# Performance work log

Measured on AMD Instinct MI355X. Metric: run time of the kernel, lower is better.

Reference implementation:

```python
import jax, jax.numpy as jnp
import numpy as np

N = 100000        # nodes
E = 1600000       # edges (avg degree 16)
IN_DIM = 128
OUT_DIM = 128
P_DROP = 0.1


def setup_inputs() -> dict:
    key = jax.random.key(0)
    k1, k2, k3, k4 = jax.random.split(key, 4)
    x = jax.random.normal(k1, (N, IN_DIM), dtype=jnp.float32)
    edge_index = jax.random.randint(k2, (2, E), 0, N, dtype=jnp.int64)
    # glorot-uniform-ish init for the GCNConv linear weight
    limit = float(np.sqrt(6.0 / (IN_DIM + OUT_DIM)))
    W = jax.random.uniform(k3, (IN_DIM, OUT_DIM), dtype=jnp.float32,
                           minval=-limit, maxval=limit)
    b = jnp.zeros((OUT_DIM,), dtype=jnp.float32)
    drop_u = jax.random.uniform(k4, (N, OUT_DIM), dtype=jnp.float32)
    return {"x": x, "edge_index": edge_index, "W": W, "b": b, "drop_u": drop_u}


def reference(x, edge_index, W, b, drop_u):
    n = x.shape[0]
    # linear transform first (PyG GCNConv: lin has no bias)
    h = x @ W  # [N, OUT]
    # add self-loops
    loops = jnp.arange(n, dtype=edge_index.dtype)
    src = jnp.concatenate([edge_index[0], loops])  # [E+N]
    dst = jnp.concatenate([edge_index[1], loops])
    # symmetric normalization: deg computed on destination column
    deg = jax.ops.segment_sum(jnp.ones_like(dst, dtype=h.dtype), dst,
                              num_segments=n)
    dinv = jnp.where(deg > 0, jax.lax.rsqrt(deg), 0.0)
    norm = dinv[src] * dinv[dst]  # [E+N]
    # gather-message-scatter: out[dst] += norm * h[src]
    msgs = h[src] * norm[:, None]                       # [E+N, OUT]
    out = jax.ops.segment_sum(msgs, dst, num_segments=n) + b
    # ReLU + (deterministic-mask) inverted dropout
    out = jax.nn.relu(out)
    keep = 1.0 - P_DROP
    out = jnp.where(drop_u >= P_DROP, out / keep, 0.0)
    return out
```

## Files before the change

### kernel.cpp

```cpp
#include <hip/hip_runtime.h>

#define DIM 128
#define D4 32
#define D2 64
#define EPB1 4096

typedef short short8 __attribute__((ext_vector_type(8)));
typedef float f32x4 __attribute__((ext_vector_type(4)));

__device__ __forceinline__ unsigned pack_bf16(float a, float b) {
    unsigned ua = __float_as_uint(a);
    unsigned ub = __float_as_uint(b);
    ua = (ua + 0x7FFFu + ((ua >> 16) & 1u)) >> 16;
    ub = (ub + 0x7FFFu + ((ub >> 16) & 1u)) & 0xFFFF0000u;
    return ua | ub;
}
__device__ __forceinline__ unsigned short bf16_of(float a) {
    unsigned ua = __float_as_uint(a);
    return (unsigned short)((ua + 0x7FFFu + ((ua >> 16) & 1u)) >> 16);
}
__device__ __forceinline__ float blo(unsigned u) { return __uint_as_float(u << 16); }
__device__ __forceinline__ float bhi(unsigned u) { return __uint_as_float(u & 0xFFFF0000u); }

__device__ __forceinline__ void acc8(const uint4& v,
                                     float& f0, float& f1, float& f2, float& f3,
                                     float& f4, float& f5, float& f6, float& f7) {
    f0 += blo(v.x); f1 += bhi(v.x);
    f2 += blo(v.y); f3 += bhi(v.y);
    f4 += blo(v.z); f5 += bhi(v.z);
    f6 += blo(v.w); f7 += bhi(v.w);
}


__global__ __launch_bounds__(512) void k_hist1(const int* __restrict__ dst, int E,
                                               int* __restrict__ H, int* __restrict__ tot,
                                               int NB1, int NBUCK,
                                               const float* __restrict__ W,
                                               unsigned short* __restrict__ wt) {
    if (blockIdx.x >= (unsigned)NB1) {
        int base = (blockIdx.x - NB1) * 2048 + threadIdx.x * 4;
#pragma unroll
        for (int i = 0; i < 4; ++i) {
            int o = base + i;
            if (o < DIM * DIM) {
                int j = o >> 7, k = o & 127;
                wt[o] = bf16_of(W[k * DIM + j]);
            }
        }
        return;
    }
    __shared__ int h[512];
    const int t = threadIdx.x;
    for (int i = t; i < NBUCK; i += 512) h[i] = 0;
    __syncthreads();
    const int base = blockIdx.x * EPB1;
#pragma unroll
    for (int i = 0; i < EPB1 / 512; ++i) {
        int e = base + i * 512 + t;
        if (e < E) atomicAdd(&h[dst[e] >> 9], 1);
    }
    __syncthreads();
    for (int i = t; i < NBUCK; i += 512) {
        int c = h[i];
        H[i * NB1 + blockIdx.x] = c;
        if (c) atomicAdd(&tot[i], c);
    }
}

__global__ __launch_bounds__(512) void k_scanB(int* __restrict__ H,
                                               const int* __restrict__ tot,
                                               int* __restrict__ binbase,
                                               int NB1, int NBUCK, int E) {
    __shared__ int sh[512];
    const int bin = blockIdx.x;
    const int t = threadIdx.x;

    int tv = (t < NBUCK) ? tot[t] : 0;
    sh[t] = tv;
    __syncthreads();
    for (int o = 1; o < 512; o <<= 1) {
        int x = (t >= o) ? sh[t - o] : 0;
        __syncthreads();
        sh[t] += x;
        __syncthreads();
    }
    const int mybase = sh[bin] - ((bin < NBUCK) ? tot[bin] : 0);
    if (t == bin && t < NBUCK) binbase[t] = mybase;
    if (bin == 0 && t == 0) binbase[NBUCK] = E;
    __syncthreads();

    int v = (t < NB1) ? H[bin * NB1 + t] : 0;
    sh[t] = v;
    __syncthreads();
    for (int o = 1; o < 512; o <<= 1) {
        int x = (t >= o) ? sh[t - o] : 0;
        __syncthreads();
        sh[t] += x;
        __syncthreads();
    }
    if (t < NB1) H[bin * NB1 + t] = mybase + sh[t] - v;
}

__global__ __launch_bounds__(512) void k_scatter1(const int* __restrict__ ei, int E,
                                                  const int* __restrict__ H,
                                                  unsigned* __restrict__ ebuf,
                                                  int NB1, int NBUCK) {
    __shared__ int cnt[512];
    const int t = threadIdx.x;
    const int blk = blockIdx.x;
    for (int i = t; i < NBUCK; i += 512) cnt[i] = 0;
    __syncthreads();
    const int* src = ei;
    const int* dst = ei + E;
    const int base = blk * EPB1;
#pragma unroll
    for (int i = 0; i < EPB1 / 512; ++i) {
        int e = base + i * 512 + t;
        if (e < E) {
            int d = dst[e];
            int s = src[e];
            int b = d >> 9;
            int r = atomicAdd(&cnt[b], 1);
            ebuf[H[b * NB1 + blk] + r] = ((unsigned)s << 9) | (unsigned)(d & 511);
        }
    }
}

__global__ __launch_bounds__(512) void k_bucket2(const unsigned* __restrict__ ebuf,
                                                 const int* __restrict__ binbase,
                                                 int* __restrict__ srclist,
                                                 int* __restrict__ rowstart,
                                                 float* __restrict__ dinv,
                                                 int n, int E) {
    __shared__ int h[512];
    __shared__ int off[512];
    __shared__ int cnt[512];
    const int t = threadIdx.x;
    const int b = blockIdx.x;
    const int beg = binbase[b];
    const int end = binbase[b + 1];
    h[t] = 0; cnt[t] = 0;
    __syncthreads();
    for (int j = beg + t; j < end; j += 512) atomicAdd(&h[ebuf[j] & 511], 1);
    __syncthreads();
    int v = h[t];
    off[t] = v;
    __syncthreads();
    for (int o = 1; o < 512; o <<= 1) {
        int x = (t >= o) ? off[t - o] : 0;
        __syncthreads();
        off[t] += x;
        __syncthreads();
    }
    const int excl = off[t] - v;
    const int node = b * 512 + t;
    if (node < n) {
        rowstart[node] = beg + excl;
        dinv[node] = rsqrtf((float)(v + 1));
    }
    if (b == 0 && t == 0) rowstart[n] = E;
    h[t] = beg + excl;
    __syncthreads();
    for (int j = beg + t; j < end; j += 512) {
        unsigned p = ebuf[j];
        int lo = p & 511;
        int r = atomicAdd(&cnt[lo], 1);
        srclist[h[lo] + r] = (int)(p >> 9);
    }
}


__global__ __launch_bounds__(256) void k_xprep(const float* __restrict__ x,
                                               const float* __restrict__ dinv,
                                               unsigned* __restrict__ xs, int n) {
    long t = (long)blockIdx.x * blockDim.x + threadIdx.x;
    long total = (long)n * D4;
    if (t >= total) return;
    int row = (int)(t >> 5);
    float di = dinv[row];
    float4 v = ((const float4*)x)[t];
    uint2 o;
    o.x = pack_bf16(v.x * di, v.y * di);
    o.y = pack_bf16(v.z * di, v.w * di);
    ((uint2*)xs)[t] = o;
}

__global__ __launch_bounds__(256) void k_wprep(const float* __restrict__ W,
                                               unsigned short* __restrict__ wt) {
    int o = blockIdx.x * blockDim.x + threadIdx.x;
    if (o >= DIM * DIM) return;
    int j = o >> 7, k = o & 127;
    wt[o] = bf16_of(W[k * DIM + j]);
}

__global__ __launch_bounds__(256) void k_gather_bb(const int* __restrict__ rowstart,
                                                   const int* __restrict__ srclist,
                                                   const uint4* __restrict__ xs4,
                                                   const float* __restrict__ dinv,
                                                   uint4* __restrict__ agg4, int n) {
    const int node = blockIdx.x * 4 + (threadIdx.x >> 6);
    const int lane = threadIdx.x & 63;
    if (node >= n) return;
    const int g = lane >> 4;
    const int q = lane & 15;
    const float di = dinv[node];

    float f0 = 0.f, f1 = 0.f, f2 = 0.f, f3 = 0.f,
          f4 = 0.f, f5 = 0.f, f6 = 0.f, f7 = 0.f;
    if (g == 0) {
        uint4 v = xs4[(long)node * 16 + q];
        acc8(v, f0, f1, f2, f3, f4, f5, f6, f7);
    }

    const int beg = rowstart[node];
    const int end = rowstart[node + 1];
    for (int base = beg; base < end; base += 64) {
        const int m = (end - base < 64) ? (end - base) : 64;
        int sidx = (base + lane < end) ? srclist[base + lane] : 0;
        int k = 0;
        for (; k + 8 <= m; k += 8) {
            int sa = __shfl(sidx, k + g);
            int sb = __shfl(sidx, k + 4 + g);
            uint4 va = xs4[(long)sa * 16 + q];
            uint4 vb = xs4[(long)sb * 16 + q];
            acc8(va, f0, f1, f2, f3, f4, f5, f6, f7);
            acc8(vb, f0, f1, f2, f3, f4, f5, f6, f7);
        }
        for (; k + 4 <= m; k += 4) {
            int sa = __shfl(sidx, k + g);
            uint4 va = xs4[(long)sa * 16 + q];
            acc8(va, f0, f1, f2, f3, f4, f5, f6, f7);
        }
        const int rem = m - k;
        if (rem) {
            int sa = __shfl(sidx, k + g);
            if (g < rem) {
                uint4 va = xs4[(long)sa * 16 + q];
                acc8(va, f0, f1, f2, f3, f4, f5, f6, f7);
            }
        }
    }

#pragma unroll
    for (int off = 16; off < 64; off <<= 1) {
        f0 += __shfl_xor(f0, off); f1 += __shfl_xor(f1, off);
        f2 += __shfl_xor(f2, off); f3 += __shfl_xor(f3, off);
        f4 += __shfl_xor(f4, off); f5 += __shfl_xor(f5, off);
        f6 += __shfl_xor(f6, off); f7 += __shfl_xor(f7, off);
    }
    if (g == 0) {
        uint4 o;
        o.x = pack_bf16(f0 * di, f1 * di);
        o.y = pack_bf16(f2 * di, f3 * di);
        o.z = pack_bf16(f4 * di, f5 * di);
        o.w = pack_bf16(f6 * di, f7 * di);
        agg4[(long)node * 16 + q] = o;
    }
}

__global__ __launch_bounds__(256) void k_mfma_transform(
        const unsigned short* __restrict__ A,
        const unsigned short* __restrict__ WT,
        const float* __restrict__ bias,
        const float* __restrict__ du,
        float* __restrict__ out, int n, int ntiles) {
    const int wave  = threadIdx.x >> 6;
    const int lane  = threadIdx.x & 63;
    const int rhalf = wave >> 1;
    const int cg    = wave & 1;
    const int lr    = lane & 15;
    const int g     = lane >> 4;
    const int lk8   = g * 8;

    const int t = blockIdx.x;
    if (t >= ntiles) return;
    const long row0 = (long)t * 32 + rhalf * 16;
    const long grow = row0 + lr;

    long ar = grow; if (ar >= n) ar = n - 1;
    short8 afr[4];
#pragma unroll
    for (int ks = 0; ks < 4; ++ks)
        afr[ks] = *reinterpret_cast<const short8*>(A + ar * DIM + ks * 32 + lk8);

    const float inv_keep = 1.0f / 0.9f;
#pragma unroll
    for (int ct = 0; ct < 4; ++ct) {
        const int colbase = cg * 64 + ct * 16;
        f32x4 acc = {0.f, 0.f, 0.f, 0.f};
#pragma unroll
        for (int ks = 0; ks < 4; ++ks) {
            short8 wfr = *reinterpret_cast<const short8*>(
                WT + (long)(colbase + lr) * DIM + ks * 32 + lk8);
            acc = __builtin_amdgcn_mfma_f32_16x16x32_bf16(wfr, afr[ks], acc, 0, 0, 0);
        }
        if (grow < n) {
            const int gcol = colbase + g * 4;
            float4 bb = *reinterpret_cast<const float4*>(bias + gcol);
            float4 u  = *reinterpret_cast<const float4*>(du + grow * DIM + gcol);
            float4 v;
            v.x = acc[0] + bb.x; v.y = acc[1] + bb.y;
            v.z = acc[2] + bb.z; v.w = acc[3] + bb.w;
            v.x = (u.x >= 0.1f) ? fmaxf(v.x, 0.f) * inv_keep : 0.f;
            v.y = (u.y >= 0.1f) ? fmaxf(v.y, 0.f) * inv_keep : 0.f;
            v.z = (u.z >= 0.1f) ? fmaxf(v.z, 0.f) * inv_keep : 0.f;
            v.w = (u.w >= 0.1f) ? fmaxf(v.w, 0.f) * inv_keep : 0.f;
            *reinterpret_cast<float4*>(out + grow * DIM + gcol) = v;
        }
    }
}


__global__ void k_hist(const int* __restrict__ dst, int E, int* __restrict__ hist) {
    int e = blockIdx.x * blockDim.x + threadIdx.x;
    if (e < E) atomicAdd(&hist[dst[e]], 1);
}
__global__ void k_dinv(const int* __restrict__ hist, float* __restrict__ dinv, int n) {
    int i = blockIdx.x * blockDim.x + threadIdx.x;
    if (i < n) dinv[i] = rsqrtf((float)(hist[i] + 1));
}
__global__ __launch_bounds__(256) void k_scan1(const int* __restrict__ hist,
                                               int* __restrict__ rowstart,
                                               int* __restrict__ bsum, int n) {
    __shared__ int sh[256];
    const int t = threadIdx.x;
    const int base = blockIdx.x * 1024 + t * 4;
    int v0 = (base + 0 < n) ? hist[base + 0] : 0;
    int v1 = (base + 1 < n) ? hist[base + 1] : 0;
    int v2 = (base + 2 < n) ? hist[base + 2] : 0;
    int v3 = (base + 3 < n) ? hist[base + 3] : 0;
    int s = v0 + v1 + v2 + v3;
    sh[t] = s;
    __syncthreads();
    for (int off = 1; off < 256; off <<= 1) {
        int xv = (t >= off) ? sh[t - off] : 0;
        __syncthreads();
        sh[t] += xv;
        __syncthreads();
    }
    if (t == 255) bsum[blockIdx.x] = sh[255];
    int run = sh[t] - s;
    if (base + 0 < n) rowstart[base + 0] = run; run += v0;
    if (base + 1 < n) rowstart[base + 1] = run; run += v1;
    if (base + 2 < n) rowstart[base + 2] = run; run += v2;
    if (base + 3 < n) rowstart[base + 3] = run;
}
__global__ __launch_bounds__(256) void k_scan2(int* __restrict__ bsum, int B) {
    __shared__ int sh[256];
    const int t = threadIdx.x;
    int v = (t < B) ? bsum[t] : 0;
    sh[t] = v;
    __syncthreads();
    for (int off = 1; off < 256; off <<= 1) {
        int xv = (t >= off) ? sh[t - off] : 0;
        __syncthreads();
        sh[t] += xv;
        __syncthreads();
    }
    if (t < B) bsum[t] = sh[t] - v;
}
__global__ void k_scan3(int* __restrict__ rowstart, const int* __restrict__ bsum,
                        int n, int E) {
    int i = blockIdx.x * blockDim.x + threadIdx.x;
    if (i < n) rowstart[i] += bsum[i >> 10];
    else if (i == n) rowstart[n] = E;
}
__global__ void k_fill(const int* __restrict__ ei, int E,
                       const int* __restrict__ rowstart, int* __restrict__ cursor,
                       int* __restrict__ srclist) {
    int e = blockIdx.x * blockDim.x + threadIdx.x;
    if (e >= E) return;
    int d = ei[E + e];
    int pos = atomicAdd(&cursor[d], 1);
    srclist[rowstart[d] + pos] = ei[e];
}
__global__ __launch_bounds__(256) void k_gather_bf(const int* __restrict__ rowstart,
                                                   const int* __restrict__ srclist,
                                                   const unsigned* __restrict__ xs,
                                                   const float* __restrict__ dinv,
                                                   float* __restrict__ out, int n) {
    const int node = blockIdx.x * 4 + (threadIdx.x >> 6);
    const int lane = threadIdx.x & 63;
    if (node >= n) return;
    const float di = dinv[node];
    unsigned sv = xs[(long)node * D2 + lane];
    float2 acc;
    acc.x = __uint_as_float(sv << 16);
    acc.y = __uint_as_float(sv & 0xFFFF0000u);
    const int beg = rowstart[node];
    const int end = rowstart[node + 1];
    int j = beg;
    for (; j + 3 < end; j += 4) {
        int s0 = srclist[j]; int s1 = srclist[j + 1];
        int s2 = srclist[j + 2]; int s3 = srclist[j + 3];
        unsigned v0 = xs[(long)s0 * D2 + lane];
        unsigned v1 = xs[(long)s1 * D2 + lane];
        unsigned v2 = xs[(long)s2 * D2 + lane];
        unsigned v3 = xs[(long)s3 * D2 + lane];
        acc.x += __uint_as_float(v0 << 16) + __uint_as_float(v1 << 16)
               + __uint_as_float(v2 << 16) + __uint_as_float(v3 << 16);
        acc.y += __uint_as_float(v0 & 0xFFFF0000u) + __uint_as_float(v1 & 0xFFFF0000u)
               + __uint_as_float(v2 & 0xFFFF0000u) + __uint_as_float(v3 & 0xFFFF0000u);
    }
    for (; j < end; ++j) {
        unsigned v0 = xs[(long)srclist[j] * D2 + lane];
        acc.x += __uint_as_float(v0 << 16);
        acc.y += __uint_as_float(v0 & 0xFFFF0000u);
    }
    acc.x *= di; acc.y *= di;
    ((float2*)out)[(long)node * D2 + lane] = acc;
}

extern "C" void kernel_launch(void* const* d_in, const int* in_sizes, int n_in,
                              void* d_out, int out_size, void* d_ws, size_t ws_size,
                              hipStream_t stream) {
    const float* x  = (const float*)d_in[0];
    const int*   ei = (const int*)d_in[1];
    const float* W  = (const float*)d_in[2];
    const float* b  = (const float*)d_in[3];
    const float* du = (const float*)d_in[4];
    float* out = (float*)d_out;

    const int n = in_sizes[0] / DIM;
    const int E = in_sizes[1] / 2;

    auto al = [](size_t v) { return (v + 255) & ~(size_t)255; };
    char* ws = (char*)d_ws;

    const int NBUCK = (n + 511) >> 9;
    const int NB1   = (E + EPB1 - 1) / EPB1;

    size_t o_dinv = 0;
    size_t o_rs   = o_dinv + al((size_t)n * 4);
    size_t o_src  = o_rs   + al(((size_t)n + 1) * 4);
    size_t o_xs   = o_src  + al((size_t)E * 4);
    size_t o_agg  = o_xs   + al((size_t)n * DIM * 2);
    size_t o_wt   = o_agg  + al((size_t)n * DIM * 2);
    size_t o_H    = o_wt   + al((size_t)DIM * DIM * 2);
    size_t o_tot  = o_H    + al((size_t)NBUCK * NB1 * 4);
    size_t o_bb   = o_tot  + al((size_t)NBUCK * 4);
    size_t o_ebuf = o_bb   + al(((size_t)NBUCK + 1) * 4);
    size_t need3  = o_ebuf + (size_t)E * 4;

    float* dinv     = (float*)(ws + o_dinv);
    int*   rowstart = (int*)(ws + o_rs);
    int*   srclist  = (int*)(ws + o_src);
    unsigned* xs    = (unsigned*)(ws + o_xs);
    unsigned* agg   = (unsigned*)(ws + o_agg);
    unsigned short* wt = (unsigned short*)(ws + o_wt);
    int*   H        = (int*)(ws + o_H);
    int*   tot      = (int*)(ws + o_tot);
    int*   binbase  = (int*)(ws + o_bb);
    unsigned* ebuf  = (unsigned*)(ws + o_ebuf);

    const int bs = 256;

    if (ws_size >= need3 && NBUCK <= 512 && NB1 <= 512) {
        (void)hipMemsetAsync(tot, 0, (size_t)NBUCK * 4, stream);
        k_hist1<<<NB1 + 8, 512, 0, stream>>>(ei + E, E, H, tot, NB1, NBUCK, W, wt);
        k_scanB<<<NBUCK, 512, 0, stream>>>(H, tot, binbase, NB1, NBUCK, E);
        k_scatter1<<<NB1, 512, 0, stream>>>(ei, E, H, ebuf, NB1, NBUCK);
        k_bucket2<<<NBUCK, 512, 0, stream>>>(ebuf, binbase, srclist, rowstart, dinv, n, E);

        long t_x = (long)n * D4;
        k_xprep<<<(int)((t_x + bs - 1) / bs), bs, 0, stream>>>(x, dinv, xs, n);
        k_gather_bb<<<(n + 3) / 4, 256, 0, stream>>>(rowstart, srclist,
                                                     (const uint4*)xs, dinv,
                                                     (uint4*)agg, n);
        int ntiles = (n + 31) / 32;
        k_mfma_transform<<<ntiles, 256, 0, stream>>>((const unsigned short*)agg, wt,
                                                     b, du, out, n, ntiles);
        return;
    }

    size_t f_dinv = 0;
    size_t f_hist = f_dinv + al((size_t)n * 4);
    size_t f_rs   = f_hist + al((size_t)n * 4);
    size_t f_bsum = f_rs   + al(((size_t)n + 1) * 4);
    size_t f_src  = f_bsum + 1024;
    size_t f_xs   = f_src  + al((size_t)E * 4);
    size_t f_agg  = f_xs   + al((size_t)n * DIM * 2);
    size_t f_wt   = f_agg  + al((size_t)n * DIM * 2);
    size_t need1  = f_agg;
    size_t need2  = f_wt + (size_t)DIM * DIM * 2;

    float* fdinv     = (float*)(ws + f_dinv);
    int*   fhist     = (int*)(ws + f_hist);
    int*   frowstart = (int*)(ws + f_rs);
    int*   fbsum     = (int*)(ws + f_bsum);
    int*   fsrclist  = (int*)(ws + f_src);
    unsigned* fxs    = (unsigned*)(ws + f_xs);
    unsigned* fagg   = (unsigned*)(ws + f_agg);
    unsigned short* fwt = (unsigned short*)(ws + f_wt);

    const int B = (n + 1023) / 1024;
    (void)hipMemsetAsync(fhist, 0, (size_t)n * 4, stream);
    k_hist<<<(E + bs - 1) / bs, bs, 0, stream>>>(ei + E, E, fhist);
    k_dinv<<<(n + bs - 1) / bs, bs, 0, stream>>>(fhist, fdinv, n);
    k_scan1<<<B, 256, 0, stream>>>(fhist, frowstart, fbsum, n);
    k_scan2<<<1, 256, 0, stream>>>(fbsum, B);
    k_scan3<<<(n + 1 + bs - 1) / bs, bs, 0, stream>>>(frowstart, fbsum, n, E);
    (void)hipMemsetAsync(fhist, 0, (size_t)n * 4, stream);
    k_fill<<<(E + bs - 1) / bs, bs, 0, stream>>>(ei, E, frowstart, fhist, fsrclist);

    if (ws_size >= need2) {
        long t_x = (long)n * D4;
        k_xprep<<<(int)((t_x + bs - 1) / bs), bs, 0, stream>>>(x, fdinv, fxs, n);
        k_wprep<<<(DIM * DIM + bs - 1) / bs, bs, 0, stream>>>(W, fwt);
        k_gather_bb<<<(n + 3) / 4, 256, 0, stream>>>(frowstart, fsrclist,
                                                     (const uint4*)fxs, fdinv,
                                                     (uint4*)fagg, n);
        int ntiles = (n + 31) / 32;
        k_mfma_transform<<<ntiles, 256, 0, stream>>>((const unsigned short*)fagg, fwt,
                                                     b, du, out, n, ntiles);
    } else if (ws_size >= need1) {
        long t_x = (long)n * D4;
        k_xprep<<<(int)((t_x + bs - 1) / bs), bs, 0, stream>>>(x, fdinv, fxs, n);
        k_gather_bf<<<(n + 3) / 4, 256, 0, stream>>>(frowstart, fsrclist, fxs, fdinv, out, n);
    }
}
```

Measured before the change: 169.1 us.

## Fuse neighbor gather and MFMA transform into one kernel via LDS tile

```diff
diff --git a/kernel.cpp b/kernel.cpp
--- a/kernel.cpp
+++ b/kernel.cpp
@@ -193,95 +193,94 @@
     wt[o] = bf16_of(W[k * DIM + j]);
 }
 
-__global__ __launch_bounds__(256) void k_gather_bb(const int* __restrict__ rowstart,
-                                                   const int* __restrict__ srclist,
-                                                   const uint4* __restrict__ xs4,
-                                                   const float* __restrict__ dinv,
-                                                   uint4* __restrict__ agg4, int n) {
-    const int node = blockIdx.x * 4 + (threadIdx.x >> 6);
+__global__ __launch_bounds__(256) void k_gather_mfma(
+        const int* __restrict__ rowstart, const int* __restrict__ srclist,
+        const uint4* __restrict__ xs4, const float* __restrict__ dinv,
+        const unsigned short* __restrict__ WT, const float* __restrict__ bias,
+        const float* __restrict__ du, float* __restrict__ out,
+        int n, int ntiles) {
+    __shared__ unsigned char Atile[32 * 256];
+
+    const int wv   = threadIdx.x >> 6;
     const int lane = threadIdx.x & 63;
-    if (node >= n) return;
     const int g = lane >> 4;
     const int q = lane & 15;
-    const float di = dinv[node];
-
-    float f0 = 0.f, f1 = 0.f, f2 = 0.f, f3 = 0.f,
-          f4 = 0.f, f5 = 0.f, f6 = 0.f, f7 = 0.f;
-    if (g == 0) {
-        uint4 v = xs4[(long)node * 16 + q];
-        acc8(v, f0, f1, f2, f3, f4, f5, f6, f7);
-    }
-
-    const int beg = rowstart[node];
-    const int end = rowstart[node + 1];
-    for (int base = beg; base < end; base += 64) {
-        const int m = (end - base < 64) ? (end - base) : 64;
-        int sidx = (base + lane < end) ? srclist[base + lane] : 0;
-        int k = 0;
-        for (; k + 8 <= m; k += 8) {
-            int sa = __shfl(sidx, k + g);
-            int sb = __shfl(sidx, k + 4 + g);
-            uint4 va = xs4[(long)sa * 16 + q];
-            uint4 vb = xs4[(long)sb * 16 + q];
-            acc8(va, f0, f1, f2, f3, f4, f5, f6, f7);
-            acc8(vb, f0, f1, f2, f3, f4, f5, f6, f7);
-        }
-        for (; k + 4 <= m; k += 4) {
-            int sa = __shfl(sidx, k + g);
-            uint4 va = xs4[(long)sa * 16 + q];
-            acc8(va, f0, f1, f2, f3, f4, f5, f6, f7);
-        }
-        const int rem = m - k;
-        if (rem) {
-            int sa = __shfl(sidx, k + g);
-            if (g < rem) {
-                uint4 va = xs4[(long)sa * 16 + q];
-                acc8(va, f0, f1, f2, f3, f4, f5, f6, f7);
+    const long row0 = (long)blockIdx.x * 32;
+
+    for (int nd = 0; nd < 8; ++nd) {
+        const int lrow = wv * 8 + nd;
+        const long node = row0 + lrow;
+        unsigned char* dstb = Atile + lrow * 256 + ((q * 16) ^ ((lrow & 7) << 4));
+        if (node < n) {
+            const float di = dinv[node];
+            float f0 = 0.f, f1 = 0.f, f2 = 0.f, f3 = 0.f,
+                  f4 = 0.f, f5 = 0.f, f6 = 0.f, f7 = 0.f;
+            if (g == 0) {
+                uint4 v = xs4[node * 16 + q];
+                acc8(v, f0, f1, f2, f3, f4, f5, f6, f7);
             }
-        }
-    }
-
-#pragma unroll
-    for (int off = 16; off < 64; off <<= 1) {
-        f0 += __shfl_xor(f0, off); f1 += __shfl_xor(f1, off);
-        f2 += __shfl_xor(f2, off); f3 += __shfl_xor(f3, off);
-        f4 += __shfl_xor(f4, off); f5 += __shfl_xor(f5, off);
-        f6 += __shfl_xor(f6, off); f7 += __shfl_xor(f7, off);
-    }
-    if (g == 0) {
-        uint4 o;
-        o.x = pack_bf16(f0 * di, f1 * di);
-        o.y = pack_bf16(f2 * di, f3 * di);
-        o.z = pack_bf16(f4 * di, f5 * di);
-        o.w = pack_bf16(f6 * di, f7 * di);
-        agg4[(long)node * 16 + q] = o;
-    }
-}
-
-__global__ __launch_bounds__(256) void k_mfma_transform(
-        const unsigned short* __restrict__ A,
-        const unsigned short* __restrict__ WT,
-        const float* __restrict__ bias,
-        const float* __restrict__ du,
-        float* __restrict__ out, int n, int ntiles) {
-    const int wave  = threadIdx.x >> 6;
-    const int lane  = threadIdx.x & 63;
-    const int rhalf = wave >> 1;
-    const int cg    = wave & 1;
+            const int beg = rowstart[node];
+            const int end = rowstart[node + 1];
+            for (int base = beg; base < end; base += 64) {
+                const int m = (end - base < 64) ? (end - base) : 64;
+                int sidx = (base + lane < end) ? srclist[base + lane] : 0;
+                int k = 0;
+                for (; k + 8 <= m; k += 8) {
+                    int sa = __shfl(sidx, k + g);
+                    int sb = __shfl(sidx, k + 4 + g);
+                    uint4 va = xs4[(long)sa * 16 + q];
+                    uint4 vb = xs4[(long)sb * 16 + q];
+                    acc8(va, f0, f1, f2, f3, f4, f5, f6, f7);
+                    acc8(vb, f0, f1, f2, f3, f4, f5, f6, f7);
+                }
+                for (; k + 4 <= m; k += 4) {
+                    int sa = __shfl(sidx, k + g);
+                    uint4 va = xs4[(long)sa * 16 + q];
+                    acc8(va, f0, f1, f2, f3, f4, f5, f6, f7);
+                }
+                const int rem = m - k;
+                if (rem) {
+                    int sa = __shfl(sidx, k + g);
+                    if (g < rem) {
+                        uint4 va = xs4[(long)sa * 16 + q];
+                        acc8(va, f0, f1, f2, f3, f4, f5, f6, f7);
+                    }
+                }
+            }
+#pragma unroll
+            for (int off = 16; off < 64; off <<= 1) {
+                f0 += __shfl_xor(f0, off); f1 += __shfl_xor(f1, off);
+                f2 += __shfl_xor(f2, off); f3 += __shfl_xor(f3, off);
+                f4 += __shfl_xor(f4, off); f5 += __shfl_xor(f5, off);
+                f6 += __shfl_xor(f6, off); f7 += __shfl_xor(f7, off);
+            }
+            if (g == 0) {
+                uint4 o;
+                o.x = pack_bf16(f0 * di, f1 * di);
+                o.y = pack_bf16(f2 * di, f3 * di);
+                o.z = pack_bf16(f4 * di, f5 * di);
+                o.w = pack_bf16(f6 * di, f7 * di);
+                *(uint4*)dstb = o;
+            }
+        } else if (g == 0) {
+            uint4 z; z.x = z.y = z.z = z.w = 0u;
+            *(uint4*)dstb = z;
+        }
+    }
+    __syncthreads();
+
+    const int rhalf = wv >> 1;
+    const int cg    = wv & 1;
     const int lr    = lane & 15;
-    const int g     = lane >> 4;
     const int lk8   = g * 8;
-
-    const int t = blockIdx.x;
-    if (t >= ntiles) return;
-    const long row0 = (long)t * 32 + rhalf * 16;
-    const long grow = row0 + lr;
-
-    long ar = grow; if (ar >= n) ar = n - 1;
+    const int lrowA = rhalf * 16 + lr;
+    const long grow = row0 + lrowA;
+
     short8 afr[4];
 #pragma unroll
     for (int ks = 0; ks < 4; ++ks)
-        afr[ks] = *reinterpret_cast<const short8*>(A + ar * DIM + ks * 32 + lk8);
+        afr[ks] = *(const short8*)(Atile + lrowA * 256 +
+                                   (((ks * 64) + g * 16) ^ ((lrowA & 7) << 4)));
 
     const float inv_keep = 1.0f / 0.9f;
 #pragma unroll
@@ -411,6 +410,119 @@
     ((float2*)out)[(long)node * D2 + lane] = acc;
 }
 
+__global__ __launch_bounds__(256) void k_gather_bb(const int* __restrict__ rowstart,
+                                                   const int* __restrict__ srclist,
+                                                   const uint4* __restrict__ xs4,
+                                                   const float* __restrict__ dinv,
+                                                   uint4* __restrict__ agg4, int n) {
+    const int node = blockIdx.x * 4 + (threadIdx.x >> 6);
+    const int lane = threadIdx.x & 63;
+    if (node >= n) return;
+    const int g = lane >> 4;
+    const int q = lane & 15;
+    const float di = dinv[node];
+
+    float f0 = 0.f, f1 = 0.f, f2 = 0.f, f3 = 0.f,
+          f4 = 0.f, f5 = 0.f, f6 = 0.f, f7 = 0.f;
+    if (g == 0) {
+        uint4 v = xs4[(long)node * 16 + q];
+        acc8(v, f0, f1, f2, f3, f4, f5, f6, f7);
+    }
+    const int beg = rowstart[node];
+    const int end = rowstart[node + 1];
+    for (int base = beg; base < end; base += 64) {
+        const int m = (end - base < 64) ? (end - base) : 64;
+        int sidx = (base + lane < end) ? srclist[base + lane] : 0;
+        int k = 0;
+        for (; k + 8 <= m; k += 8) {
+            int sa = __shfl(sidx, k + g);
+            int sb = __shfl(sidx, k + 4 + g);
+            uint4 va = xs4[(long)sa * 16 + q];
+            uint4 vb = xs4[(long)sb * 16 + q];
+            acc8(va, f0, f1, f2, f3, f4, f5, f6, f7);
+            acc8(vb, f0, f1, f2, f3, f4, f5, f6, f7);
+        }
+        for (; k + 4 <= m; k += 4) {
+            int sa = __shfl(sidx, k + g);
+            uint4 va = xs4[(long)sa * 16 + q];
+            acc8(va, f0, f1, f2, f3, f4, f5, f6, f7);
+        }
+        const int rem = m - k;
+        if (rem) {
+            int sa = __shfl(sidx, k + g);
+            if (g < rem) {
+                uint4 va = xs4[(long)sa * 16 + q];
+                acc8(va, f0, f1, f2, f3, f4, f5, f6, f7);
+            }
+        }
+    }
+#pragma unroll
+    for (int off = 16; off < 64; off <<= 1) {
+        f0 += __shfl_xor(f0, off); f1 += __shfl_xor(f1, off);
+        f2 += __shfl_xor(f2, off); f3 += __shfl_xor(f3, off);
+        f4 += __shfl_xor(f4, off); f5 += __shfl_xor(f5, off);
+        f6 += __shfl_xor(f6, off); f7 += __shfl_xor(f7, off);
+    }
+    if (g == 0) {
+        uint4 o;
+        o.x = pack_bf16(f0 * di, f1 * di);
+        o.y = pack_bf16(f2 * di, f3 * di);
+        o.z = pack_bf16(f4 * di, f5 * di);
+        o.w = pack_bf16(f6 * di, f7 * di);
+        agg4[(long)node * 16 + q] = o;
+    }
+}
+
+__global__ __launch_bounds__(256) void k_mfma_transform(
+        const unsigned short* __restrict__ A, const unsigned short* __restrict__ WT,
+        const float* __restrict__ bias, const float* __restrict__ du,
+        float* __restrict__ out, int n, int ntiles) {
+    const int wave  = threadIdx.x >> 6;
+    const int lane  = threadIdx.x & 63;
+    const int rhalf = wave >> 1;
+    const int cg    = wave & 1;
+    const int lr    = lane & 15;
+    const int g     = lane >> 4;
+    const int lk8   = g * 8;
+
+    const int t = blockIdx.x;
+    if (t >= ntiles) return;
+    const long row0 = (long)t * 32 + rhalf * 16;
+    const long grow = row0 + lr;
+
+    long ar = grow; if (ar >= n) ar = n - 1;
+    short8 afr[4];
+#pragma unroll
+    for (int ks = 0; ks < 4; ++ks)
+        afr[ks] = *reinterpret_cast<const short8*>(A + ar * DIM + ks * 32 + lk8);
+
+    const float inv_keep = 1.0f / 0.9f;
+#pragma unroll
+    for (int ct = 0; ct < 4; ++ct) {
+        const int colbase = cg * 64 + ct * 16;
+        f32x4 acc = {0.f, 0.f, 0.f, 0.f};
+#pragma unroll
+        for (int ks = 0; ks < 4; ++ks) {
+            short8 wfr = *reinterpret_cast<const short8*>(
+                WT + (long)(colbase + lr) * DIM + ks * 32 + lk8);
+            acc = __builtin_amdgcn_mfma_f32_16x16x32_bf16(wfr, afr[ks], acc, 0, 0, 0);
+        }
+        if (grow < n) {
+            const int gcol = colbase + g * 4;
+            float4 bb = *reinterpret_cast<const float4*>(bias + gcol);
+            float4 u  = *reinterpret_cast<const float4*>(du + grow * DIM + gcol);
+            float4 v;
+            v.x = acc[0] + bb.x; v.y = acc[1] + bb.y;
+            v.z = acc[2] + bb.z; v.w = acc[3] + bb.w;
+            v.x = (u.x >= 0.1f) ? fmaxf(v.x, 0.f) * inv_keep : 0.f;
+            v.y = (u.y >= 0.1f) ? fmaxf(v.y, 0.f) * inv_keep : 0.f;
+            v.z = (u.z >= 0.1f) ? fmaxf(v.z, 0.f) * inv_keep : 0.f;
+            v.w = (u.w >= 0.1f) ? fmaxf(v.w, 0.f) * inv_keep : 0.f;
+            *reinterpret_cast<float4*>(out + grow * DIM + gcol) = v;
+        }
+    }
+}
+
 extern "C" void kernel_launch(void* const* d_in, const int* in_sizes, int n_in,
                               void* d_out, int out_size, void* d_ws, size_t ws_size,
                               hipStream_t stream) {
@@ -464,12 +576,10 @@
 
         long t_x = (long)n * D4;
         k_xprep<<<(int)((t_x + bs - 1) / bs), bs, 0, stream>>>(x, dinv, xs, n);
-        k_gather_bb<<<(n + 3) / 4, 256, 0, stream>>>(rowstart, srclist,
-                                                     (const uint4*)xs, dinv,
-                                                     (uint4*)agg, n);
         int ntiles = (n + 31) / 32;
-        k_mfma_transform<<<ntiles, 256, 0, stream>>>((const unsigned short*)agg, wt,
-                                                     b, du, out, n, ntiles);
+        k_gather_mfma<<<ntiles, 256, 0, stream>>>(rowstart, srclist,
+                                                  (const uint4*)xs, dinv,
+                                                  wt, b, du, out, n, ntiles);
         return;
     }
 
```

After: 158.5 us. 1.07x faster.
